# Kernel tuning notes

Hardware: AMD Instinct MI355X
Metric: run time of the kernel (lower is better)

Reference implementation:

```python
import jax, jax.numpy as jnp
import numpy as np
import math

B, S, D, H, HD, P = 2, 2048, 2048, 16, 128, 10
ROPE_BASE = 10000.0


def _rope_tables(seq_len, head_dim):
    inv_freq = 1.0 / (ROPE_BASE ** (np.arange(0, head_dim, 2, dtype=np.float32) / head_dim))
    t = np.arange(seq_len, dtype=np.float32)
    freqs = np.outer(t, inv_freq)                  # [S, hd/2]
    emb = np.concatenate([freqs, freqs], axis=-1)  # [S, hd]
    return jnp.asarray(np.cos(emb)), jnp.asarray(np.sin(emb))


def _rotate_half(x):
    half = x.shape[-1] // 2
    return jnp.concatenate([-x[..., half:], x[..., :half]], axis=-1)


def setup_inputs() -> dict:
    key = jax.random.key(0)
    ks = jax.random.split(key, 8)
    hidden_states = jax.random.normal(ks[0], (B, S, D), dtype=jnp.float32)
    # causal additive mask, llama convention: 0 where allowed, large negative above diagonal
    causal = jnp.triu(jnp.full((S, S), -1e9, dtype=jnp.float32), k=1)
    attention_mask = jnp.broadcast_to(causal[None, None], (B, 1, S, S))
    position_ids = jnp.broadcast_to(jnp.arange(S, dtype=jnp.int64)[None], (B, S))
    scale = 1.0 / math.sqrt(D)
    Wq = jax.random.normal(ks[1], (D, D), dtype=jnp.float32) * scale
    Wk = jax.random.normal(ks[2], (D, D), dtype=jnp.float32) * scale
    Wv = jax.random.normal(ks[3], (D, D), dtype=jnp.float32) * scale
    Wo = jax.random.normal(ks[4], (D, D), dtype=jnp.float32) * scale
    adapter_query = jax.random.normal(ks[5], (P, D), dtype=jnp.float32)
    adapter_gate = jax.random.normal(ks[6], (1, H, 1, 1), dtype=jnp.float32) * 0.1
    return dict(hidden_states=hidden_states, attention_mask=attention_mask,
                position_ids=position_ids, Wq=Wq, Wk=Wk, Wv=Wv, Wo=Wo,
                adapter_query=adapter_query, adapter_gate=adapter_gate)


def reference(hidden_states, attention_mask, position_ids, Wq, Wk, Wv, Wo,
              adapter_query, adapter_gate):
    bsz, q_len, _ = hidden_states.shape
    inv_sqrt_hd = 1.0 / math.sqrt(HD)

    def split_heads(x):  # [B,S,D] -> [B,H,S,hd]
        return x.reshape(bsz, q_len, H, HD).transpose(0, 2, 1, 3)

    q = split_heads(hidden_states @ Wq)
    k = split_heads(hidden_states @ Wk)
    v = split_heads(hidden_states @ Wv)

    # RoPE
    cos_t, sin_t = _rope_tables(q_len, HD)
    cos = cos_t[position_ids][:, None]  # [B,1,S,hd]
    sin = sin_t[position_ids][:, None]
    q = q * cos + _rotate_half(q) * sin
    k = k * cos + _rotate_half(k) * sin

    # main attention
    scores = jnp.einsum('bhqd,bhkd->bhqk', q, k) * inv_sqrt_hd
    scores = scores + attention_mask
    attn = jax.nn.softmax(scores.astype(jnp.float32), axis=-1).astype(q.dtype)
    attn_out = jnp.einsum('bhqk,bhkd->bhqd', attn, v)

    # adapter: soft prompt projected through k/v proj (learn_kv=False), no RoPE
    adapter = jnp.broadcast_to(adapter_query[None], (bsz, P, D))  # [B,P,D]
    a_k = (adapter @ Wk).reshape(bsz, P, H, HD).transpose(0, 2, 1, 3)  # [B,H,P,hd]
    a_v = (adapter @ Wv).reshape(bsz, P, H, HD).transpose(0, 2, 1, 3)
    a_scores = jnp.einsum('bhqd,bhpd->bhqp', q, a_k) * inv_sqrt_hd
    a_w = adapter_gate * jax.nn.softmax(a_scores.astype(jnp.float32), axis=-1).astype(q.dtype)
    a_out = jnp.einsum('bhqp,bhpd->bhqd', a_w, a_v)

    out = attn_out + a_out
    out = out.transpose(0, 2, 1, 3).reshape(bsz, q_len, D)
    return out @ Wo
```

## Files before the change

kernel.cpp:

```cpp
#include <hip/hip_runtime.h>
#include <cstdint>
#include <cstddef>

typedef __bf16 bf16x8 __attribute__((ext_vector_type(8)));
typedef float  f32x4  __attribute__((ext_vector_type(4)));

__device__ __forceinline__ unsigned short f2bf(float f) {
  unsigned int u = __float_as_uint(f);
  u += 0x7FFF + ((u >> 16) & 1);
  return (unsigned short)(u >> 16);
}
__device__ __forceinline__ float bf2f(unsigned short u) {
  return __uint_as_float(((unsigned int)u) << 16);
}

#define SEQ 2048
#define DMODEL 2048
#define NH 16
#define HD 128
#define NB 2
#define NP 10
#define MAUG 4106
#define SCALEL2 (0.08838834764831845f * 1.44269504088896340f)

#define GLOAD_LDS16(g, l) \
  __builtin_amdgcn_global_load_lds((__attribute__((address_space(1))) const void*)(g), \
                                   (__attribute__((address_space(3))) void*)(l), 16, 0, 0)

#define FENCE() asm volatile("" ::: "memory")
#define SBAR() do { FENCE(); __builtin_amdgcn_s_barrier(); FENCE(); } while (0)
#define WAITVM(N) asm volatile("s_waitcnt vmcnt(" #N ")" ::: "memory")

__global__ void k_tables(float* __restrict__ cost, float* __restrict__ sint) {
  int idx = blockIdx.x * 256 + threadIdx.x;
  if (idx >= SEQ * 64) return;
  int s = idx >> 6, i = idx & 63;
  double invf = exp(-((double)(2 * i) / 128.0) * log(10000.0));
  double a = (double)s * invf;
  float c = (float)cos(a), sn = (float)sin(a);
  cost[s * HD + i] = c;  cost[s * HD + 64 + i] = c;
  sint[s * HD + i] = sn; sint[s * HD + 64 + i] = sn;
}

__global__ __launch_bounds__(256) void k_wt(const float* __restrict__ W0,
                                            const float* __restrict__ W1,
                                            const float* __restrict__ W2,
                                            const float* __restrict__ W3,
                                            unsigned short* __restrict__ out) {
  __shared__ float tile[32][33];
  const float* W = (blockIdx.z == 0) ? W0 : (blockIdx.z == 1) ? W1 : (blockIdx.z == 2) ? W2 : W3;
  unsigned short* o = out + (size_t)blockIdx.z * DMODEL * DMODEL;
  int bx = blockIdx.x * 32, by = blockIdx.y * 32;
  int tx = threadIdx.x & 31, ty = threadIdx.x >> 5;
  #pragma unroll
  for (int j = 0; j < 32; j += 8)
    tile[ty + j][tx] = W[(size_t)(bx + ty + j) * DMODEL + by + tx];
  __syncthreads();
  #pragma unroll
  for (int j = 0; j < 32; j += 8)
    o[(size_t)(by + ty + j) * DMODEL + bx + tx] = f2bf(tile[tx][ty + j]);
}

__global__ void k_xaug(const float* __restrict__ X, const float* __restrict__ Aq,
                       unsigned short* __restrict__ xaug) {
  size_t idx = (size_t)blockIdx.x * 256 + threadIdx.x;
  if (idx >= (size_t)MAUG * DMODEL) return;
  size_t row = idx >> 11;
  int col = (int)(idx & 2047);
  float v = (row < (size_t)NB * SEQ) ? X[idx] : Aq[(row - NB * SEQ) * DMODEL + col];
  xaug[idx] = f2bf(v);
}

#define LDA_HALF(MH) do { \
  _Pragma("unroll") for (int i_ = 0; i_ < 4; i_++) \
    _Pragma("unroll") for (int ks_ = 0; ks_ < 2; ks_++) \
      a[i_][ks_] = *(const bf16x8*)&lds[base + (wr*128 + (MH)*64 + i_*16 + lr)*64 + (((ks_*4+quad) ^ (lr & 7)) * 8)]; \
} while (0)

#define LDB_PAIR(NHH) do { \
  _Pragma("unroll") for (int j_ = 0; j_ < 2; j_++) \
    _Pragma("unroll") for (int ks_ = 0; ks_ < 2; ks_++) \
      b[(NHH)*2+j_][ks_] = *(const bf16x8*)&lds[base + 16384 + (wc*64 + ((NHH)*2+j_)*16 + lr)*64 + (((ks_*4+quad) ^ (lr & 7)) * 8)]; \
} while (0)

#define MFMA_QUAD(MH, NHH) do { \
  __builtin_amdgcn_s_setprio(1); \
  _Pragma("unroll") for (int i_ = 0; i_ < 4; i_++) \
    _Pragma("unroll") for (int j_ = 0; j_ < 2; j_++) { \
      acc[(MH)*4+i_][(NHH)*2+j_] = __builtin_amdgcn_mfma_f32_16x16x32_bf16(a[i_][0], b[(NHH)*2+j_][0], acc[(MH)*4+i_][(NHH)*2+j_], 0, 0, 0); \
      acc[(MH)*4+i_][(NHH)*2+j_] = __builtin_amdgcn_mfma_f32_16x16x32_bf16(a[i_][1], b[(NHH)*2+j_][1], acc[(MH)*4+i_][(NHH)*2+j_], 0, 0, 0); \
    } \
  __builtin_amdgcn_s_setprio(0); \
} while (0)

#define STG_AE(nb, ko) do { \
  GLOAD_LDS16(sA + (ko),                      &lds[(nb)*32768 + (qrow)*64 + g8]); \
  GLOAD_LDS16(sA + 128*(size_t)DMODEL + (ko), &lds[(nb)*32768 + (128+qrow)*64 + g8]); } while (0)
#define STG_AO(nb, ko) do { \
  GLOAD_LDS16(sA + 64*(size_t)DMODEL + (ko),  &lds[(nb)*32768 + (64+qrow)*64 + g8]); \
  GLOAD_LDS16(sA + 192*(size_t)DMODEL + (ko), &lds[(nb)*32768 + (192+qrow)*64 + g8]); } while (0)
#define STG_BE(nb, ko) do { \
  GLOAD_LDS16(sB + (ko),                      &lds[(nb)*32768 + 16384 + (qb)*64 + g8]); \
  GLOAD_LDS16(sB + 128*(size_t)DMODEL + (ko), &lds[(nb)*32768 + 16384 + (128+qb)*64 + g8]); } while (0)
#define STG_BO(nb, ko) do { \
  GLOAD_LDS16(sB + 32*(size_t)DMODEL + (ko),  &lds[(nb)*32768 + 16384 + (32+qb)*64 + g8]); \
  GLOAD_LDS16(sB + 160*(size_t)DMODEL + (ko), &lds[(nb)*32768 + 16384 + (160+qb)*64 + g8]); } while (0)

template<int BF16OUT>
__global__ __launch_bounds__(512, 2) void k_gemm256(const unsigned short* __restrict__ A,
                                                    const unsigned short* __restrict__ Bt,
                                                    void* __restrict__ Cv,
                                                    int M, size_t c_stride_mat) {
  __shared__ unsigned short lds[65536];
  const int t = threadIdx.x;
  const int lane = t & 63, w = t >> 6;
  const int lr = lane & 15, quad = lane >> 4;
  const int wr = w >> 2, wc = w & 3;
  const int tm = (M + 255) >> 8;
  const int perz = tm * 8;
  const int qchunk = gridDim.x >> 3;
  const int lin = (blockIdx.x & 7) * qchunk + (blockIdx.x >> 3);
  const int z = lin / perz;
  const int rem = lin - z * perz;
  const int m0 = (rem >> 3) * 256, n0 = (rem & 7) * 256;
  const unsigned short* Bz = Bt + (size_t)z * DMODEL * DMODEL;

  const int qrow = t >> 3;
  const int g8 = (t & 7) * 8;
  const int gsw8 = (((t & 7) ^ (qrow & 7)) * 8);
  const int qb = (qrow < 32) ? qrow : qrow + 32;

  const unsigned short* sA = A + (size_t)(m0 + qrow) * DMODEL + gsw8;
  const unsigned short* sB = Bz + (size_t)(n0 + qb) * DMODEL + gsw8;

  bf16x8 a[4][2], b[4][2];
  f32x4 acc[8][4];
  #pragma unroll
  for (int i = 0; i < 8; i++)
    #pragma unroll
    for (int j = 0; j < 4; j++) acc[i][j] = (f32x4){0.f, 0.f, 0.f, 0.f};

  STG_AE(0, 0); STG_BE(0, 0); STG_BO(0, 0); STG_AO(0, 0);
  WAITVM(4);
  SBAR();

  for (int kt = 0; kt < DMODEL / 64; kt++) {
    const int base = (kt & 1) << 15;
    const int nb = (kt & 1) ^ 1;
    const int ko = (kt + 1) * 64;
    const bool more = (kt + 1 < DMODEL / 64);

    LDA_HALF(0);
    LDB_PAIR(0);
    if (more) STG_AE(nb, ko);
    SBAR();
    MFMA_QUAD(0, 0);
    if (more) WAITVM(4); else WAITVM(2);
    SBAR();

    LDB_PAIR(1);
    if (more) STG_BE(nb, ko);
    SBAR();
    MFMA_QUAD(0, 1);
    if (more) WAITVM(4); else WAITVM(0);
    SBAR();

    LDA_HALF(1);
    if (more) STG_BO(nb, ko);
    SBAR();
    MFMA_QUAD(1, 0);
    SBAR();

    if (more) STG_AO(nb, ko);
    SBAR();
    MFMA_QUAD(1, 1);
    if (more) WAITVM(4);
    SBAR();
  }

  #pragma unroll
  for (int mi = 0; mi < 8; mi++) {
    #pragma unroll
    for (int r = 0; r < 4; r++) {
      int row = m0 + wr * 128 + mi * 16 + quad * 4 + r;
      if (row < M) {
        if (BF16OUT) {
          unsigned short* C = (unsigned short*)Cv + (size_t)z * c_stride_mat;
          #pragma unroll
          for (int n = 0; n < 4; n++)
            C[(size_t)row * DMODEL + n0 + wc * 64 + n * 16 + lr] = f2bf(acc[mi][n][r]);
        } else {
          float* C = (float*)Cv + (size_t)z * c_stride_mat;
          #pragma unroll
          for (int n = 0; n < 4; n++)
            C[(size_t)row * DMODEL + n0 + wc * 64 + n * 16 + lr] = acc[mi][n][r];
        }
      }
    }
  }
}

#define O_LDA(MH) do { \
  _Pragma("unroll") for (int i_ = 0; i_ < 2; i_++) \
    _Pragma("unroll") for (int ks_ = 0; ks_ < 2; ks_++) \
      a[i_][ks_] = *(const bf16x8*)&lds[base + (wr*64 + ((MH)*2+i_)*16 + lr)*64 + (((ks_*4+quad) ^ (lr & 7)) * 8)]; \
} while (0)

#define O_LDB(NHH) do { \
  _Pragma("unroll") for (int j_ = 0; j_ < 2; j_++) \
    _Pragma("unroll") for (int ks_ = 0; ks_ < 2; ks_++) \
      b[(NHH)*2+j_][ks_] = *(const bf16x8*)&lds[base + 8192 + (wc*64 + ((NHH)*2+j_)*16 + lr)*64 + (((ks_*4+quad) ^ (lr & 7)) * 8)]; \
} while (0)

#define O_MFMA(MH, NHH) do { \
  __builtin_amdgcn_s_setprio(1); \
  _Pragma("unroll") for (int i_ = 0; i_ < 2; i_++) \
    _Pragma("unroll") for (int j_ = 0; j_ < 2; j_++) { \
      acc[(MH)*2+i_][(NHH)*2+j_] = __builtin_amdgcn_mfma_f32_16x16x32_bf16(a[i_][0], b[(NHH)*2+j_][0], acc[(MH)*2+i_][(NHH)*2+j_], 0, 0, 0); \
      acc[(MH)*2+i_][(NHH)*2+j_] = __builtin_amdgcn_mfma_f32_16x16x32_bf16(a[i_][1], b[(NHH)*2+j_][1], acc[(MH)*2+i_][(NHH)*2+j_], 0, 0, 0); \
    } \
  __builtin_amdgcn_s_setprio(0); \
} while (0)

#define O_STG_AE(nb, ko) GLOAD_LDS16(sA + (ko), &lds[(nb)*24576 + (qb)*64 + g8])
#define O_STG_AO(nb, ko) GLOAD_LDS16(sA + 32*(size_t)DMODEL + (ko), &lds[(nb)*24576 + (32+qb)*64 + g8])
#define O_STG_BE(nb, ko) do { \
  GLOAD_LDS16(sB + (ko),                      &lds[(nb)*24576 + 8192 + (qb)*64 + g8]); \
  GLOAD_LDS16(sB + 128*(size_t)DMODEL + (ko), &lds[(nb)*24576 + 8192 + (128+qb)*64 + g8]); } while (0)
#define O_STG_BO(nb, ko) do { \
  GLOAD_LDS16(sB + 32*(size_t)DMODEL + (ko),  &lds[(nb)*24576 + 8192 + (32+qb)*64 + g8]); \
  GLOAD_LDS16(sB + 160*(size_t)DMODEL + (ko), &lds[(nb)*24576 + 8192 + (160+qb)*64 + g8]); } while (0)

__global__ __launch_bounds__(512, 2) void k_gemmo(const unsigned short* __restrict__ A,
                                                  const unsigned short* __restrict__ Bt,
                                                  float* __restrict__ C) {
  __shared__ unsigned short lds[49152];
  const int t = threadIdx.x;
  const int lane = t & 63, w = t >> 6;
  const int lr = lane & 15, quad = lane >> 4;
  const int wr = w >> 2, wc = w & 3;
  const int lin = (blockIdx.x & 7) * 32 + (blockIdx.x >> 3);
  const int m0 = (lin >> 3) * 128, n0 = (lin & 7) * 256;

  const int qrow = t >> 3;
  const int g8 = (t & 7) * 8;
  const int gsw8 = (((t & 7) ^ (qrow & 7)) * 8);
  const int qb = (qrow < 32) ? qrow : qrow + 32;

  const unsigned short* sA = A + (size_t)(m0 + qb) * DMODEL + gsw8;
  const unsigned short* sB = Bt + (size_t)(n0 + qb) * DMODEL + gsw8;

  bf16x8 a[2][2], b[4][2];
  f32x4 acc[4][4];
  #pragma unroll
  for (int i = 0; i < 4; i++)
    #pragma unroll
    for (int j = 0; j < 4; j++) acc[i][j] = (f32x4){0.f, 0.f, 0.f, 0.f};

  O_STG_AE(0, 0); O_STG_BE(0, 0); O_STG_BO(0, 0); O_STG_AO(0, 0);
  WAITVM(3);
  SBAR();

  for (int kt = 0; kt < DMODEL / 64; kt++) {
    const int base = (kt & 1) * 24576;
    const int nb = (kt & 1) ^ 1;
    const int ko = (kt + 1) * 64;
    const bool more = (kt + 1 < DMODEL / 64);

    O_LDA(0);
    O_LDB(0);
    if (more) O_STG_AE(nb, ko);
    SBAR();
    O_MFMA(0, 0);
    if (more) WAITVM(2); else WAITVM(1);
    SBAR();

    O_LDB(1);
    if (more) O_STG_BE(nb, ko);
    SBAR();
    O_MFMA(0, 1);
    if (more) WAITVM(3); else WAITVM(0);
    SBAR();

    O_LDA(1);
    if (more) O_STG_BO(nb, ko);
    SBAR();
    O_MFMA(1, 0);
    SBAR();

    if (more) O_STG_AO(nb, ko);
    SBAR();
    O_MFMA(1, 1);
    if (more) WAITVM(3);
    SBAR();
  }

  #pragma unroll
  for (int mi = 0; mi < 4; mi++) {
    #pragma unroll
    for (int r = 0; r < 4; r++) {
      int row = m0 + wr * 64 + mi * 16 + quad * 4 + r;
      #pragma unroll
      for (int n = 0; n < 4; n++)
        C[(size_t)row * DMODEL + n0 + wc * 64 + n * 16 + lr] = acc[mi][n][r];
    }
  }
}

__global__ __launch_bounds__(256) void k_rope(const unsigned short* __restrict__ Qf,
                                              const unsigned short* __restrict__ Kf,
                                              const unsigned short* __restrict__ Vf,
                                              const float* __restrict__ cost, const float* __restrict__ sint,
                                              unsigned short* __restrict__ Qb, unsigned short* __restrict__ Kb,
                                              unsigned short* __restrict__ AKb, unsigned short* __restrict__ avt) {
  int row = blockIdx.x;
  int t = threadIdx.x;
  int c0 = t * 8;
  size_t off = (size_t)row * DMODEL + c0;
  if (row < NB * SEQ) {
    int s = row & (SEQ - 1);
    int d0 = c0 & (HD - 1);
    int po = (d0 < 64) ? 64 : -64;
    float sign = (d0 < 64) ? -1.f : 1.f;
    uint4 qv = *(const uint4*)&Qf[off];
    uint4 qp = *(const uint4*)&Qf[off + po];
    uint4 kv = *(const uint4*)&Kf[off];
    uint4 kp = *(const uint4*)&Kf[off + po];
    const unsigned short* qa = (const unsigned short*)&qv;
    const unsigned short* qb2 = (const unsigned short*)&qp;
    const unsigned short* ka = (const unsigned short*)&kv;
    const unsigned short* kb2 = (const unsigned short*)&kp;
    unsigned short oq[8], ok[8];
    #pragma unroll
    for (int j = 0; j < 8; j++) {
      float cv = cost[s * HD + d0 + j], sv = sint[s * HD + d0 + j];
      oq[j] = f2bf(bf2f(qa[j]) * cv + sign * bf2f(qb2[j]) * sv);
      ok[j] = f2bf(bf2f(ka[j]) * cv + sign * bf2f(kb2[j]) * sv);
    }
    *(uint4*)&Qb[off] = *(const uint4*)oq;
    *(uint4*)&Kb[off] = *(const uint4*)ok;
  } else {
    int p = row - NB * SEQ;
    uint4 kv = *(const uint4*)&Kf[off];
    uint4 vv = *(const uint4*)&Vf[off];
    *(uint4*)&AKb[(size_t)p * DMODEL + c0] = kv;
    const unsigned short* vp = (const unsigned short*)&vv;
    #pragma unroll
    for (int j = 0; j < 8; j++)
      avt[(size_t)(c0 + j) * 32 + p] = vp[j];
  }
}

__global__ __launch_bounds__(256) void k_vt(const unsigned short* __restrict__ Vf,
                                            unsigned short* __restrict__ Vt) {
  __shared__ unsigned short tile[64][72];
  const int t = threadIdx.x;
  int s0 = blockIdx.x * 64;
  int d0 = blockIdx.y * 64;
  int b = blockIdx.z >> 4, h = blockIdx.z & 15;
  #pragma unroll
  for (int j = t; j < 512; j += 256) {
    int row = j >> 3, ch = j & 7;
    *(uint4*)&tile[row][ch * 8] =
      *(const uint4*)&Vf[(size_t)(b * SEQ + s0 + row) * DMODEL + h * HD + d0 + ch * 8];
  }
  __syncthreads();
  #pragma unroll
  for (int j = t; j < 512; j += 256) {
    int dr = j >> 3, ch = j & 7;
    unsigned short tmp[8];
    #pragma unroll
    for (int k = 0; k < 8; k++) tmp[k] = tile[ch * 8 + k][dr];
    *(uint4*)&Vt[((size_t)((b * NH + h) * HD + d0 + dr)) * SEQ + s0 + ch * 8] = *(const uint4*)tmp;
  }
}

#define PSTR 68

__global__ __launch_bounds__(256, 3) void k_flash(const unsigned short* __restrict__ Qb,
                                               const unsigned short* __restrict__ Kb,
                                               const unsigned short* __restrict__ Vt,
                                               const unsigned short* __restrict__ AKb,
                                               const unsigned short* __restrict__ avt,
                                               const float* __restrict__ gate,
                                               unsigned short* __restrict__ Obuf,
                                               float* __restrict__ ml,
                                               unsigned short* __restrict__ Aout) {
  const int L = blockIdx.x;
  const int h = L & 15;
  const int slot = 39 - (L >> 4);
  const int b = blockIdx.y;
  int qt, j, P;
  if (slot < 4)       { qt = slot;               j = 0;          P = 1; }
  else if (slot < 12) { int s = slot - 4;  qt = 4 + (s >> 1);  j = s & 1; P = 2; }
  else if (slot < 24) { int s = slot - 12; qt = 8 + s / 3;     j = s % 3; P = 3; }
  else                { int s = slot - 24; qt = 12 + (s >> 2); j = s & 3; P = 4; }

  const int t = threadIdx.x, w = t >> 6, lane = t & 63;
  const int lr = lane & 15, quad = lane >> 4;

  __shared__ unsigned short Ks[64 * 128];
  __shared__ unsigned short Vs[128 * 64];
  __shared__ unsigned short Ps[4][32 * PSTR];
  unsigned short* Ps16 = &Ps[w][0];

  const int row_base = qt * 128 + w * 32;

  bf16x8 qf[2][4];
  #pragma unroll
  for (int mt = 0; mt < 2; mt++)
    #pragma unroll
    for (int kk = 0; kk < 4; kk++)
      qf[mt][kk] = *(const bf16x8*)&Qb[((size_t)(b * SEQ + row_base + mt * 16 + lr)) * DMODEL
                                       + h * HD + kk * 32 + quad * 8];

  f32x4 o[2][8];
  #pragma unroll
  for (int mt = 0; mt < 2; mt++)
    #pragma unroll
    for (int nt = 0; nt < 8; nt++) o[mt][nt] = (f32x4){0.f, 0.f, 0.f, 0.f};
  float l_i[2][4];
  #pragma unroll
  for (int mt = 0; mt < 2; mt++)
    #pragma unroll
    for (int r = 0; r < 4; r++) l_i[mt][r] = 0.f;

  const int krow = t >> 4;
  const int vd = t >> 3, vc = (t & 7) ^ (vd & 7);
  const int ktend = 2 * qt + 2;

  for (int kt = j; kt < ktend; kt += P) {
    __syncthreads();
    #pragma unroll
    for (int jj = 0; jj < 4; jj++) {
      int row = krow + jj * 16;
      int c = (t & 15) ^ (row & 15);
      GLOAD_LDS16(&Kb[((size_t)(b * SEQ + kt * 64 + row)) * DMODEL + h * HD + c * 8],
                  &Ks[(t + jj * 256) * 8]);
    }
    #pragma unroll
    for (int jj = 0; jj < 4; jj++) {
      int d = vd + jj * 32;
      GLOAD_LDS16(&Vt[((size_t)((b * NH + h) * HD + d)) * SEQ + kt * 64 + vc * 8],
                  &Vs[(t + jj * 256) * 8]);
    }
    __syncthreads();

    f32x4 s4[2][4];
    #pragma unroll
    for (int mt = 0; mt < 2; mt++)
      #pragma unroll
      for (int nt = 0; nt < 4; nt++) s4[mt][nt] = (f32x4){0.f, 0.f, 0.f, 0.f};
    #pragma unroll
    for (int nt = 0; nt < 4; nt++)
      #pragma unroll
      for (int kk = 0; kk < 4; kk++) {
        bf16x8 bv = *(const bf16x8*)&Ks[((nt * 16 + lr) * 16 + ((kk * 4 + quad) ^ lr)) * 8];
        s4[0][nt] = __builtin_amdgcn_mfma_f32_16x16x32_bf16(qf[0][kk], bv, s4[0][nt], 0, 0, 0);
        s4[1][nt] = __builtin_amdgcn_mfma_f32_16x16x32_bf16(qf[1][kk], bv, s4[1][nt], 0, 0, 0);
      }

    const int maybe_mask = (kt * 64 + 63 > row_base);
    #pragma unroll
    for (int mt = 0; mt < 2; mt++) {
      #pragma unroll
      for (int nt = 0; nt < 4; nt++) s4[mt][nt] = s4[mt][nt] * SCALEL2;
      if (maybe_mask) {
        #pragma unroll
        for (int nt = 0; nt < 4; nt++) {
          int col = kt * 64 + nt * 16 + lr;
          #pragma unroll
          for (int r = 0; r < 4; r++)
            if (col > row_base + mt * 16 + quad * 4 + r) s4[mt][nt][r] = -__builtin_inff();
        }
      }
      #pragma unroll
      for (int nt = 0; nt < 4; nt++)
        #pragma unroll
        for (int r = 0; r < 4; r++) {
          float p = __builtin_amdgcn_exp2f(s4[mt][nt][r]);
          l_i[mt][r] += p;
          Ps[w][(mt * 16 + quad * 4 + r) * PSTR + nt * 16 + lr] = f2bf(p);
        }
    }
    #pragma unroll
    for (int kk2 = 0; kk2 < 2; kk2++) {
      bf16x8 af0 = *(const bf16x8*)&Ps[w][(lr) * PSTR + kk2 * 32 + quad * 8];
      bf16x8 af1 = *(const bf16x8*)&Ps[w][(16 + lr) * PSTR + kk2 * 32 + quad * 8];
      #pragma unroll
      for (int nt = 0; nt < 8; nt++) {
        bf16x8 bv = *(const bf16x8*)&Vs[((nt * 16 + lr) * 8 + ((kk2 * 4 + quad) ^ (lr & 7))) * 8];
        o[0][nt] = __builtin_amdgcn_mfma_f32_16x16x32_bf16(af0, bv, o[0][nt], 0, 0, 0);
        o[1][nt] = __builtin_amdgcn_mfma_f32_16x16x32_bf16(af1, bv, o[1][nt], 0, 0, 0);
      }
    }
  }

  #pragma unroll
  for (int mt = 0; mt < 2; mt++)
    #pragma unroll
    for (int r = 0; r < 4; r++) {
      float l = l_i[mt][r];
      #pragma unroll
      for (int off = 1; off < 16; off <<= 1) l += __shfl_xor(l, off, 64);
      l_i[mt][r] = l;
    }

  const size_t slotg = (size_t)(b * 16 + h) * 40 + slot;

  if (j == 0) {
    const float g = gate[h];
    #pragma unroll
    for (int mt = 0; mt < 2; mt++) {
      f32x4 as4 = (f32x4){0.f, 0.f, 0.f, 0.f};
      #pragma unroll
      for (int kk = 0; kk < 4; kk++) {
        bf16x8 akf = *(const bf16x8*)&AKb[(size_t)lr * DMODEL + h * HD + kk * 32 + quad * 8];
        as4 = __builtin_amdgcn_mfma_f32_16x16x32_bf16(qf[mt][kk], akf, as4, 0, 0, 0);
      }
      as4 = as4 * SCALEL2;
      float al[4];
      #pragma unroll
      for (int r = 0; r < 4; r++) {
        float p = (lr < NP) ? __builtin_amdgcn_exp2f(as4[r]) : 0.f;
        as4[r] = p;
        float sum = p;
        #pragma unroll
        for (int off = 1; off < 16; off <<= 1) sum += __shfl_xor(sum, off, 64);
        al[r] = sum;
      }
      #pragma unroll
      for (int r = 0; r < 4; r++) {
        Ps[w][(mt * 16 + quad * 4 + r) * PSTR + lr] = f2bf(as4[r]);
        Ps[w][(mt * 16 + quad * 4 + r) * PSTR + 16 + lr] = 0;
      }
      bf16x8 af = *(const bf16x8*)&Ps[w][(mt * 16 + lr) * PSTR + quad * 8];
      f32x4 pa[8];
      #pragma unroll
      for (int nt = 0; nt < 8; nt++) {
        bf16x8 bv = *(const bf16x8*)&avt[(size_t)(h * HD + nt * 16 + lr) * 32 + quad * 8];
        pa[nt] = __builtin_amdgcn_mfma_f32_16x16x32_bf16(af, bv, (f32x4){0.f, 0.f, 0.f, 0.f}, 0, 0, 0);
      }
      float invla[4];
      #pragma unroll
      for (int r = 0; r < 4; r++) invla[r] = g / al[r];
      #pragma unroll
      for (int nt = 0; nt < 8; nt++)
        #pragma unroll
        for (int r = 0; r < 4; r++)
          Ps16[(quad * 4 + r) * 128 + nt * 16 + lr] = f2bf(pa[nt][r] * invla[r]);
      size_t gb = (((size_t)(b * 16 + h) * 16 + qt)) * 16384 + (size_t)(w * 32 + mt * 16) * 128;
      #pragma unroll
      for (int it = 0; it < 4; it++) {
        int i = lane + it * 64;
        int rr = i >> 4, ch = i & 15;
        *(uint4*)&Aout[gb + rr * 128 + ch * 8] = *(const uint4*)&Ps16[rr * 128 + ch * 8];
      }
    }
  }

  #pragma unroll
  for (int mt = 0; mt < 2; mt++) {
    if (lr == 0) {
      #pragma unroll
      for (int r = 0; r < 4; r++) {
        int rl = w * 32 + mt * 16 + quad * 4 + r;
        ml[slotg * 128 + rl] = l_i[mt][r];
      }
    }
    #pragma unroll
    for (int nt = 0; nt < 8; nt++)
      #pragma unroll
      for (int r = 0; r < 4; r++)
        Ps16[(quad * 4 + r) * 128 + nt * 16 + lr] = f2bf(o[mt][nt][r]);
    size_t gb = slotg * 16384 + (size_t)(w * 32 + mt * 16) * 128;
    #pragma unroll
    for (int it = 0; it < 4; it++) {
      int i = lane + it * 64;
      int rr = i >> 4, ch = i & 15;
      *(uint4*)&Obuf[gb + rr * 128 + ch * 8] = *(const uint4*)&Ps16[rr * 128 + ch * 8];
    }
  }
}

__global__ __launch_bounds__(256) void k_merge(const unsigned short* __restrict__ Obuf,
                                               const float* __restrict__ ml,
                                               const unsigned short* __restrict__ Aout,
                                               unsigned short* __restrict__ ab) {
  int idx = blockIdx.x * 256 + threadIdx.x;
  int ch = idx & 15;
  int row = (idx >> 4) & 2047;
  int h = (idx >> 15) & 15;
  int b = idx >> 19;
  int qt = row >> 7, rl = row & 127;
  int start = qt < 4 ? qt : qt < 8 ? 4 + 2 * (qt - 4) : qt < 12 ? 12 + 3 * (qt - 8) : 24 + 4 * (qt - 12);
  int P = qt < 4 ? 1 : qt < 8 ? 2 : qt < 12 ? 3 : 4;
  size_t sbase = (size_t)(b * 16 + h) * 40 + start;
  float den = 0.f;
  float acc[8] = {0.f, 0.f, 0.f, 0.f, 0.f, 0.f, 0.f, 0.f};
  #pragma unroll
  for (int jp = 0; jp < 4; jp++) {
    if (jp < P) {
      den += ml[(sbase + jp) * 128 + rl];
      uint4 ov = *(const uint4*)&Obuf[(sbase + jp) * 16384 + rl * 128 + ch * 8];
      const unsigned short* pv = (const unsigned short*)&ov;
      #pragma unroll
      for (int k = 0; k < 8; k++) acc[k] += bf2f(pv[k]);
    }
  }
  uint4 av = *(const uint4*)&Aout[(((size_t)(b * 16 + h) * 16 + qt)) * 16384 + rl * 128 + ch * 8];
  const unsigned short* pa = (const unsigned short*)&av;
  float dn = 1.0f / den;
  unsigned short res[8];
  #pragma unroll
  for (int k = 0; k < 8; k++) res[k] = f2bf(acc[k] * dn + bf2f(pa[k]));
  *(uint4*)&ab[((size_t)(b * 2048 + row)) * 2048 + h * 128 + ch * 8] = *(const uint4*)res;
}

extern "C" void kernel_launch(void* const* d_in, const int* in_sizes, int n_in,
                              void* d_out, int out_size, void* d_ws, size_t ws_size,
                              hipStream_t stream) {
  const float* hidden = (const float*)d_in[0];
  const float* Wq = (const float*)d_in[3];
  const float* Wk = (const float*)d_in[4];
  const float* Wv = (const float*)d_in[5];
  const float* Wo = (const float*)d_in[6];
  const float* Aq = (const float*)d_in[7];
  const float* gate = (const float*)d_in[8];
  float* out = (float*)d_out;

  char* ws = (char*)d_ws;
  size_t off = 0;
  auto alloc = [&](size_t bytes) -> void* {
    void* p = ws + off;
    off = (off + bytes + 255) & ~(size_t)255;
    return p;
  };
  unsigned short* wt   = (unsigned short*)alloc((size_t)4 * DMODEL * DMODEL * 2);
  unsigned short* xaug = (unsigned short*)alloc((size_t)MAUG * DMODEL * 2);
  unsigned short* qkvb = (unsigned short*)alloc((size_t)3 * MAUG * DMODEL * 2);
  unsigned short* qf = qkvb;
  unsigned short* kf = qkvb + (size_t)MAUG * DMODEL;
  unsigned short* vf = kf + (size_t)MAUG * DMODEL;
  unsigned short* qb  = (unsigned short*)alloc((size_t)NB * SEQ * DMODEL * 2);
  unsigned short* kb  = (unsigned short*)alloc((size_t)NB * SEQ * DMODEL * 2);
  unsigned short* vt  = (unsigned short*)alloc((size_t)NB * SEQ * DMODEL * 2);
  unsigned short* akb = (unsigned short*)alloc((size_t)16 * DMODEL * 2);
  unsigned short* avt = (unsigned short*)alloc((size_t)DMODEL * 32 * 2);
  float* cost = (float*)alloc((size_t)SEQ * HD * 4);
  float* sint = (float*)alloc((size_t)SEQ * HD * 4);
  unsigned short* obuf = (unsigned short*)alloc((size_t)NB * NH * 40 * 16384 * 2);
  float* mlb = (float*)alloc((size_t)NB * NH * 40 * 128 * 4);
  unsigned short* aout = (unsigned short*)alloc((size_t)NB * NH * 16 * 16384 * 2);
  unsigned short* ab = qf;

  k_tables<<<SEQ * 64 / 256, 256, 0, stream>>>(cost, sint);
  k_wt<<<dim3(64, 64, 4), 256, 0, stream>>>(Wq, Wk, Wv, Wo, wt);
  {
    size_t n = (size_t)MAUG * DMODEL;
    k_xaug<<<(unsigned)((n + 255) / 256), 256, 0, stream>>>(hidden, Aq, xaug);
  }
  k_gemm256<1><<<dim3(408), 512, 0, stream>>>(xaug, wt, qkvb, MAUG, (size_t)MAUG * DMODEL);
  hipMemsetAsync(avt, 0, (size_t)DMODEL * 32 * 2, stream);
  k_rope<<<MAUG, 256, 0, stream>>>(qf, kf, vf, cost, sint, qb, kb, akb, avt);
  k_vt<<<dim3(32, 2, 32), 256, 0, stream>>>(vf, vt);
  k_flash<<<dim3(640, 2), 256, 0, stream>>>(qb, kb, vt, akb, avt, gate, obuf, mlb, aout);
  k_merge<<<4096, 256, 0, stream>>>(obuf, mlb, aout, ab);
  k_gemmo<<<dim3(256), 512, 0, stream>>>(ab, wt + (size_t)3 * DMODEL * DMODEL, out);
}
```

Baseline: 468.7 us.

## Double-buffer register fragments and cut barriers in GEMM main loops

Restructures the K-loop of both the projection GEMM and output GEMM so A/B fragments are held in separate even/odd register sets. The next tile's first fragments are read from LDS at the end of each iteration, overlapping with the last MFMA block. This reduces the number of workgroup barriers per iteration from eight to about three, removing synchronization stalls between LDS reads and MFMAs. It raises register pressure and tightens the ordering constraints on global-to-LDS staging versus LDS reads.

Result: no change. 466.8 us (-0.4%).

```diff
diff --git a/kernel.cpp b/kernel.cpp
--- a/kernel.cpp
+++ b/kernel.cpp
@@ -71,24 +71,24 @@
   xaug[idx] = f2bf(v);
 }
 
-#define LDA_HALF(MH) do { \
+#define RD_A(dst, bb, MH) do { \
   _Pragma("unroll") for (int i_ = 0; i_ < 4; i_++) \
     _Pragma("unroll") for (int ks_ = 0; ks_ < 2; ks_++) \
-      a[i_][ks_] = *(const bf16x8*)&lds[base + (wr*128 + (MH)*64 + i_*16 + lr)*64 + (((ks_*4+quad) ^ (lr & 7)) * 8)]; \
+      dst[i_][ks_] = *(const bf16x8*)&lds[(bb) + (wr*128 + (MH)*64 + i_*16 + lr)*64 + (((ks_*4+quad) ^ (lr & 7)) * 8)]; \
 } while (0)
 
-#define LDB_PAIR(NHH) do { \
+#define RD_B(dst, bb, NHH) do { \
   _Pragma("unroll") for (int j_ = 0; j_ < 2; j_++) \
     _Pragma("unroll") for (int ks_ = 0; ks_ < 2; ks_++) \
-      b[(NHH)*2+j_][ks_] = *(const bf16x8*)&lds[base + 16384 + (wc*64 + ((NHH)*2+j_)*16 + lr)*64 + (((ks_*4+quad) ^ (lr & 7)) * 8)]; \
+      dst[j_][ks_] = *(const bf16x8*)&lds[(bb) + 16384 + (wc*64 + (NHH)*32 + j_*16 + lr)*64 + (((ks_*4+quad) ^ (lr & 7)) * 8)]; \
 } while (0)
 
-#define MFMA_QUAD(MH, NHH) do { \
+#define MM(A, B, MH, NHH) do { \
   __builtin_amdgcn_s_setprio(1); \
   _Pragma("unroll") for (int i_ = 0; i_ < 4; i_++) \
     _Pragma("unroll") for (int j_ = 0; j_ < 2; j_++) { \
-      acc[(MH)*4+i_][(NHH)*2+j_] = __builtin_amdgcn_mfma_f32_16x16x32_bf16(a[i_][0], b[(NHH)*2+j_][0], acc[(MH)*4+i_][(NHH)*2+j_], 0, 0, 0); \
-      acc[(MH)*4+i_][(NHH)*2+j_] = __builtin_amdgcn_mfma_f32_16x16x32_bf16(a[i_][1], b[(NHH)*2+j_][1], acc[(MH)*4+i_][(NHH)*2+j_], 0, 0, 0); \
+      acc[(MH)*4+i_][(NHH)*2+j_] = __builtin_amdgcn_mfma_f32_16x16x32_bf16(A[i_][0], B[j_][0], acc[(MH)*4+i_][(NHH)*2+j_], 0, 0, 0); \
+      acc[(MH)*4+i_][(NHH)*2+j_] = __builtin_amdgcn_mfma_f32_16x16x32_bf16(A[i_][1], B[j_][1], acc[(MH)*4+i_][(NHH)*2+j_], 0, 0, 0); \
     } \
   __builtin_amdgcn_s_setprio(0); \
 } while (0)
@@ -133,7 +133,7 @@
   const unsigned short* sA = A + (size_t)(m0 + qrow) * DMODEL + gsw8;
   const unsigned short* sB = Bz + (size_t)(n0 + qb) * DMODEL + gsw8;
 
-  bf16x8 a[4][2], b[4][2];
+  bf16x8 aE[4][2], aO[4][2], bE[2][2], bO[2][2];
   f32x4 acc[8][4];
   #pragma unroll
   for (int i = 0; i < 8; i++)
@@ -143,39 +143,35 @@
   STG_AE(0, 0); STG_BE(0, 0); STG_BO(0, 0); STG_AO(0, 0);
   WAITVM(4);
   SBAR();
+  RD_A(aE, 0, 0); RD_B(bE, 0, 0);
 
   for (int kt = 0; kt < DMODEL / 64; kt++) {
     const int base = (kt & 1) << 15;
-    const int nb = (kt & 1) ^ 1;
+    const int nb2 = (kt & 1) ^ 1;
+    const int nbase = nb2 << 15;
     const int ko = (kt + 1) * 64;
     const bool more = (kt + 1 < DMODEL / 64);
 
-    LDA_HALF(0);
-    LDB_PAIR(0);
-    if (more) STG_AE(nb, ko);
+    if (more) { STG_AE(nb2, ko); WAITVM(4); } else WAITVM(2);
     SBAR();
-    MFMA_QUAD(0, 0);
-    if (more) WAITVM(4); else WAITVM(2);
+    RD_B(bO, base, 1);
+    MM(aE, bE, 0, 0);
+
+    if (more) { STG_BE(nb2, ko); WAITVM(4); } else WAITVM(0);
     SBAR();
-
-    LDB_PAIR(1);
-    if (more) STG_BE(nb, ko);
-    SBAR();
-    MFMA_QUAD(0, 1);
-    if (more) WAITVM(4); else WAITVM(0);
-    SBAR();
-
-    LDA_HALF(1);
-    if (more) STG_BO(nb, ko);
-    SBAR();
-    MFMA_QUAD(1, 0);
-    SBAR();
-
-    if (more) STG_AO(nb, ko);
-    SBAR();
-    MFMA_QUAD(1, 1);
-    if (more) WAITVM(4);
-    SBAR();
+    RD_A(aO, base, 1);
+    MM(aE, bO, 0, 1);
+
+    if (more) STG_BO(nb2, ko);
+    MM(aO, bE, 1, 0);
+
+    if (more) {
+      STG_AO(nb2, ko);
+      WAITVM(4);
+      SBAR();
+      RD_A(aE, nbase, 0); RD_B(bE, nbase, 0);
+    }
+    MM(aO, bO, 1, 1);
   }
 
   #pragma unroll
@@ -200,24 +196,24 @@
   }
 }
 
-#define O_LDA(MH) do { \
+#define O_RD_A(dst, bb, MH) do { \
   _Pragma("unroll") for (int i_ = 0; i_ < 2; i_++) \
     _Pragma("unroll") for (int ks_ = 0; ks_ < 2; ks_++) \
-      a[i_][ks_] = *(const bf16x8*)&lds[base + (wr*64 + ((MH)*2+i_)*16 + lr)*64 + (((ks_*4+quad) ^ (lr & 7)) * 8)]; \
+      dst[i_][ks_] = *(const bf16x8*)&lds[(bb) + (wr*64 + (MH)*32 + i_*16 + lr)*64 + (((ks_*4+quad) ^ (lr & 7)) * 8)]; \
 } while (0)
 
-#define O_LDB(NHH) do { \
+#define O_RD_B(dst, bb, NHH) do { \
   _Pragma("unroll") for (int j_ = 0; j_ < 2; j_++) \
     _Pragma("unroll") for (int ks_ = 0; ks_ < 2; ks_++) \
-      b[(NHH)*2+j_][ks_] = *(const bf16x8*)&lds[base + 8192 + (wc*64 + ((NHH)*2+j_)*16 + lr)*64 + (((ks_*4+quad) ^ (lr & 7)) * 8)]; \
+      dst[j_][ks_] = *(const bf16x8*)&lds[(bb) + 8192 + (wc*64 + (NHH)*32 + j_*16 + lr)*64 + (((ks_*4+quad) ^ (lr & 7)) * 8)]; \
 } while (0)
 
-#define O_MFMA(MH, NHH) do { \
+#define O_MM(A, B, MH, NHH) do { \
   __builtin_amdgcn_s_setprio(1); \
   _Pragma("unroll") for (int i_ = 0; i_ < 2; i_++) \
     _Pragma("unroll") for (int j_ = 0; j_ < 2; j_++) { \
-      acc[(MH)*2+i_][(NHH)*2+j_] = __builtin_amdgcn_mfma_f32_16x16x32_bf16(a[i_][0], b[(NHH)*2+j_][0], acc[(MH)*2+i_][(NHH)*2+j_], 0, 0, 0); \
-      acc[(MH)*2+i_][(NHH)*2+j_] = __builtin_amdgcn_mfma_f32_16x16x32_bf16(a[i_][1], b[(NHH)*2+j_][1], acc[(MH)*2+i_][(NHH)*2+j_], 0, 0, 0); \
+      acc[(MH)*2+i_][(NHH)*2+j_] = __builtin_amdgcn_mfma_f32_16x16x32_bf16(A[i_][0], B[j_][0], acc[(MH)*2+i_][(NHH)*2+j_], 0, 0, 0); \
+      acc[(MH)*2+i_][(NHH)*2+j_] = __builtin_amdgcn_mfma_f32_16x16x32_bf16(A[i_][1], B[j_][1], acc[(MH)*2+i_][(NHH)*2+j_], 0, 0, 0); \
     } \
   __builtin_amdgcn_s_setprio(0); \
 } while (0)
@@ -250,7 +246,7 @@
   const unsigned short* sA = A + (size_t)(m0 + qb) * DMODEL + gsw8;
   const unsigned short* sB = Bt + (size_t)(n0 + qb) * DMODEL + gsw8;
 
-  bf16x8 a[2][2], b[4][2];
+  bf16x8 aE[2][2], aO[2][2], bE[2][2], bO[2][2];
   f32x4 acc[4][4];
   #pragma unroll
   for (int i = 0; i < 4; i++)
@@ -260,39 +256,35 @@
   O_STG_AE(0, 0); O_STG_BE(0, 0); O_STG_BO(0, 0); O_STG_AO(0, 0);
   WAITVM(3);
   SBAR();
+  O_RD_A(aE, 0, 0); O_RD_B(bE, 0, 0);
 
   for (int kt = 0; kt < DMODEL / 64; kt++) {
     const int base = (kt & 1) * 24576;
-    const int nb = (kt & 1) ^ 1;
+    const int nb2 = (kt & 1) ^ 1;
+    const int nbase = nb2 * 24576;
     const int ko = (kt + 1) * 64;
     const bool more = (kt + 1 < DMODEL / 64);
 
-    O_LDA(0);
-    O_LDB(0);
-    if (more) O_STG_AE(nb, ko);
+    if (more) { O_STG_AE(nb2, ko); WAITVM(2); } else WAITVM(1);
     SBAR();
-    O_MFMA(0, 0);
-    if (more) WAITVM(2); else WAITVM(1);
+    O_RD_B(bO, base, 1);
+    O_MM(aE, bE, 0, 0);
+
+    if (more) { O_STG_BE(nb2, ko); WAITVM(3); } else WAITVM(0);
     SBAR();
-
-    O_LDB(1);
-    if (more) O_STG_BE(nb, ko);
-    SBAR();
-    O_MFMA(0, 1);
-    if (more) WAITVM(3); else WAITVM(0);
-    SBAR();
-
-    O_LDA(1);
-    if (more) O_STG_BO(nb, ko);
-    SBAR();
-    O_MFMA(1, 0);
-    SBAR();
-
-    if (more) O_STG_AO(nb, ko);
-    SBAR();
-    O_MFMA(1, 1);
-    if (more) WAITVM(3);
-    SBAR();
+    O_RD_A(aO, base, 1);
+    O_MM(aE, bO, 0, 1);
+
+    if (more) O_STG_BO(nb2, ko);
+    O_MM(aO, bE, 1, 0);
+
+    if (more) {
+      O_STG_AO(nb2, ko);
+      WAITVM(3);
+      SBAR();
+      O_RD_A(aE, nbase, 0); O_RD_B(bE, nbase, 0);
+    }
+    O_MM(aO, bO, 1, 1);
   }
 
   #pragma unroll
```
